# Optimization experiments

Measured on AMD Instinct MI355X. Metric: run time of the kernel, lower is better.

## Reference

```python
import jax, jax.numpy as jnp
import numpy as np

THETA = 10000.0
MASK_FILL = -60000.0

def _rope(x):
    # lucidrains rotary_embedding_torch semantics: interleaved pairs, full-dim rotation
    S, D = x.shape[-2], x.shape[-1]
    inv_freq = 1.0 / (THETA ** (jnp.arange(0, D, 2, dtype=jnp.float32) / D))  # [D/2]
    freqs = jnp.arange(S, dtype=jnp.float32)[:, None] * inv_freq[None, :]     # [S, D/2]
    freqs = jnp.repeat(freqs, 2, axis=-1)                                     # [S, D] (each freq twice)
    cos, sin = jnp.cos(freqs), jnp.sin(freqs)
    xr = x.reshape(x.shape[:-1] + (D // 2, 2))
    rot_half = jnp.stack((-xr[..., 1], xr[..., 0]), axis=-1).reshape(x.shape)  # (x1,x2)->(-x2,x1)
    return x * cos + rot_half * sin

def setup_inputs() -> dict:
    key = jax.random.key(0)
    kq, kk, kv, km = jax.random.split(key, 4)
    B, H, S, D = 4, 16, 2048, 128
    return {
        "query": jax.random.normal(kq, (B, H, S, D), dtype=jnp.float32),
        "key": jax.random.normal(kk, (B, H, S, D), dtype=jnp.float32),
        "value": jax.random.normal(kv, (B, H, S, D), dtype=jnp.float32),
        "mask": jax.random.randint(km, (1, 1, S, S), 0, 2, dtype=jnp.int32),
    }

def reference(query, key, value, mask):
    q = _rope(query)
    k = _rope(key)
    scale = 1.0 / jnp.sqrt(jnp.float32(q.shape[-1]))
    scores = jnp.einsum('bhqd,bhkd->bhqk', q, k) * scale
    scores = jnp.where(mask == 0, jnp.float32(MASK_FILL), scores)
    p_attn = jax.nn.softmax(scores, axis=-1)
    out = jnp.einsum('bhqk,bhkd->bhqd', p_attn, value)
    return out, p_attn
```

## Files before the change

### kernel.cpp

```cpp
#include <hip/hip_runtime.h>
#include <hip/hip_fp16.h>
#include <cstdint>
#include <cstddef>

#define Bn 4
#define Hn 16
#define Sn 2048
#define Dn 128
#define MSHIFT 8.0f

typedef _Float16 half8  __attribute__((ext_vector_type(8)));
typedef float    f32x16 __attribute__((ext_vector_type(16)));
typedef float    f32x4v __attribute__((ext_vector_type(4)));
typedef unsigned uint4v __attribute__((ext_vector_type(4)));

__device__ __forceinline__ int pk_f16(float a, float b){
  auto h = __builtin_amdgcn_cvt_pkrtz(a, b);
  return __builtin_bit_cast(int, h);
}


__global__ void k_prep0(float2* __restrict__ tab,
                        const int* __restrict__ mask, unsigned* __restrict__ mtb){
  const int bid = blockIdx.x;
  if (bid < 512){
    const int idx = bid*256 + threadIdx.x;
    const int i = idx & 63, s = idx >> 6;
    const double invf = exp(-(double)i * (9.210340371976184 / 64.0));
    const double ang  = (double)s * invf;
    float2 cs; cs.x = (float)cos(ang); cs.y = (float)sin(ang);
    tab[idx] = cs;
  } else {
    const int g = (bid - 512)*256 + threadIdx.x;
    const int k = g & (Sn-1), q32 = g >> 11;
    unsigned bits = 0u;
    for (int j = 0; j < 32; ++j)
      bits |= (mask[(size_t)(q32*32 + j)*Sn + k] != 0 ? 1u : 0u) << j;
    mtb[g] = bits;
  }
}


__global__ void k_pack(const float* __restrict__ q, const float* __restrict__ k,
                       const float* __restrict__ v, const float2* __restrict__ tab,
                       half8* __restrict__ qp, half8* __restrict__ kp,
                       half8* __restrict__ vp){
  const int bid = blockIdx.x;
  if (bid < 8192){
    const int t    = bid*256 + threadIdx.x;
    const int lane = t & 63, ln = lane & 31, h = lane >> 5;
    const int dc   = (t >> 6) & 7;
    const int blk  = (t >> 9) & 63;
    const int bh   = t >> 15;
    const int s    = blk*32 + ln;
    const size_t roff = ((size_t)bh*Sn + s)*Dn + dc*16 + h*8;
    const float4 a0 = *(const float4*)(q + roff);
    const float4 a1 = *(const float4*)(q + roff + 4);
    const float4 b0 = *(const float4*)(k + roff);
    const float4 b1 = *(const float4*)(k + roff + 4);
    const float2* tb = tab + s*64 + dc*8 + h*4;
    const float2 c0 = tb[0], c1 = tb[1], c2 = tb[2], c3 = tb[3];
    const float SC = 0.08838834764831845f;
    half8 qo, ko;
    qo[0] = (_Float16)((a0.x*c0.x - a0.y*c0.y)*SC);
    qo[1] = (_Float16)((a0.y*c0.x + a0.x*c0.y)*SC);
    qo[2] = (_Float16)((a0.z*c1.x - a0.w*c1.y)*SC);
    qo[3] = (_Float16)((a0.w*c1.x + a0.z*c1.y)*SC);
    qo[4] = (_Float16)((a1.x*c2.x - a1.y*c2.y)*SC);
    qo[5] = (_Float16)((a1.y*c2.x + a1.x*c2.y)*SC);
    qo[6] = (_Float16)((a1.z*c3.x - a1.w*c3.y)*SC);
    qo[7] = (_Float16)((a1.w*c3.x + a1.z*c3.y)*SC);
    ko[0] = (_Float16)(b0.x*c0.x - b0.y*c0.y);
    ko[1] = (_Float16)(b0.y*c0.x + b0.x*c0.y);
    ko[2] = (_Float16)(b0.z*c1.x - b0.w*c1.y);
    ko[3] = (_Float16)(b0.w*c1.x + b0.z*c1.y);
    ko[4] = (_Float16)(b1.x*c2.x - b1.y*c2.y);
    ko[5] = (_Float16)(b1.y*c2.x + b1.x*c2.y);
    ko[6] = (_Float16)(b1.z*c3.x - b1.w*c3.y);
    ko[7] = (_Float16)(b1.w*c3.x + b1.z*c3.y);
    qp[t] = qo;
    kp[t] = ko;
  } else {
    const int t    = (bid - 8192)*256 + threadIdx.x;
    const int lane = t & 63, ln = lane & 31, h = lane >> 5;
    const int dt   = (t >> 6) & 3;
    const int k16  = (t >> 8) & 127;
    const int bh   = t >> 15;
    const size_t base = ((size_t)bh*Sn + k16*16 + h*8)*Dn + dt*32 + ln;
    half8 o;
#pragma unroll
    for (int j = 0; j < 8; ++j) o[j] = (_Float16)v[base + (size_t)j*Dn];
    vp[t] = o;
  }
}


__global__ __launch_bounds__(512, 2) void attn_ps2(
    const half8* __restrict__ qp, const half8* __restrict__ kp,
    const unsigned* __restrict__ mtb, half8* __restrict__ wfrag,
    float* __restrict__ rinvb)
{
  const int bid  = blockIdx.x;
  const int work = ((bid & 7) << 6) + (bid >> 3);
  const int bh   = work >> 3;
  const int qg   = work & 7;
  const int w    = threadIdx.x >> 6;
  const int l    = threadIdx.x & 63;
  const int ln   = l & 31;
  const int h    = l >> 5;
  const int qb   = qg*8 + w;
  const int strip = bh*64 + qb;

  half8 qf[8];
#pragma unroll
  for (int dc = 0; dc < 8; ++dc)
    qf[dc] = qp[(((size_t)bh*64 + qb)*8 + dc)*64 + l];

  const unsigned* mrow = mtb + (size_t)qb*Sn;
  half8* wbase = wfrag + (size_t)strip*128*64;
  float L = 0.f;

  for (int kt = 0; kt < 64; ++kt){
    const half8* kf = kp + (((size_t)bh*64 + kt)*8)*64 + l;
    f32x16 a;
#pragma unroll
    for (int i = 0; i < 16; ++i) a[i] = 0.f;
#pragma unroll
    for (int dc = 0; dc < 8; ++dc)
      a = __builtin_amdgcn_mfma_f32_32x32x16_f16(kf[(size_t)dc*64], qf[dc], a, 0, 0, 0);

#pragma unroll
    for (int mm = 0; mm < 4; ++mm){
      const uint4v dw = *(const uint4v*)(mrow + kt*32 + mm*8 + h*4);
#pragma unroll
      for (int aa = 0; aa < 4; ++aa){
        const int r = mm*4 + aa;
        const float s = ((dw[aa] >> ln) & 1u) ? a[r] : -1.0e30f;
        const float u = __expf(s - MSHIFT);
        a[r] = u;
        L += u;
      }
    }

    int pk2[4][2];
#pragma unroll
    for (int b = 0; b < 4; ++b){
      pk2[b][0] = pk_f16(a[4*b+0], a[4*b+1]);
      pk2[b][1] = pk_f16(a[4*b+2], a[4*b+3]);
    }

#pragma unroll
    for (int t16 = 0; t16 < 2; ++t16){
      const int P00 = pk2[2*t16+0][0];
      const int P01 = pk2[2*t16+0][1];
      const int P10 = pk2[2*t16+1][0];
      const int P11 = pk2[2*t16+1][1];
      const int S00 = __shfl_xor(P00, 32, 64);
      const int S01 = __shfl_xor(P01, 32, 64);
      const int S10 = __shfl_xor(P10, 32, 64);
      const int S11 = __shfl_xor(P11, 32, 64);
      int4 bi;
      bi.x = h ? S10 : P00;
      bi.y = h ? S11 : P01;
      bi.z = h ? P10 : S00;
      bi.w = h ? P11 : S01;
      wbase[(size_t)(kt*2 + t16)*64 + l] = __builtin_bit_cast(half8, bi);
    }
  }

  L += __shfl_xor(L, 32, 64);
  if (l < 32) rinvb[(size_t)strip*32 + ln] = 1.0f / L;
}


__global__ __launch_bounds__(512, 2) void attn_ox(
    const half8* __restrict__ vp, const half8* __restrict__ wfrag,
    const float* __restrict__ rinvb, float* __restrict__ out,
    float* __restrict__ pout)
{
  __shared__ _Float16 ps[32][1032];
  __shared__ float rv[32];

  const int bid = blockIdx.x;
  const int tid = threadIdx.x;
  const int l   = tid & 63;
  const int ln  = l & 31;
  const int h   = l >> 5;

  if (bid % 17 == 0){
    const int o_id = bid / 17;
    const int work = 511 - (((o_id & 7) << 6) + (o_id >> 3));
    const int bh   = work >> 3;
    const int qg   = work & 7;
    const int w    = tid >> 6;
    const int qb   = qg*8 + w;
    const int strip = bh*64 + qb;
    float* pt = (float*)&ps[0][0];
    #define PT(W,Q,C) pt[(((W)*32 + (Q))*34) + (C)]

    f32x16 oacc[4];
#pragma unroll
    for (int dt = 0; dt < 4; ++dt)
#pragma unroll
      for (int i = 0; i < 16; ++i) oacc[dt][i] = 0.f;

    const half8* wbase = wfrag + (size_t)strip*128*64;
    const half8* vbase = vp + (size_t)bh*128*4*64;

#pragma unroll 4
    for (int ks = 0; ks < 128; ++ks){
      const half8 bf = wbase[(size_t)ks*64 + l];
      const half8* vf = vbase + (size_t)ks*4*64 + l;
#pragma unroll
      for (int dt = 0; dt < 4; ++dt)
        oacc[dt] = __builtin_amdgcn_mfma_f32_32x32x16_f16(vf[(size_t)dt*64], bf, oacc[dt], 0, 0, 0);
    }

    const float rinv = rinvb[(size_t)strip*32 + ln];
#pragma unroll
    for (int dt = 0; dt < 4; ++dt)
#pragma unroll
      for (int i = 0; i < 16; ++i) oacc[dt][i] *= rinv;

    const size_t obase = ((size_t)bh*Sn + qb*32)*Dn;
    const int rq = l >> 3;
    const int rc = (l & 7) * 4;
#pragma unroll
    for (int dt = 0; dt < 4; ++dt){
#pragma unroll
      for (int g = 0; g < 4; ++g){
        const int c = g*8 + h*4;
        float2 e0, e1;
        e0.x = oacc[dt][4*g+0]; e0.y = oacc[dt][4*g+1];
        e1.x = oacc[dt][4*g+2]; e1.y = oacc[dt][4*g+3];
        *(float2*)&PT(w, ln, c)   = e0;
        *(float2*)&PT(w, ln, c+2) = e1;
      }
#pragma unroll
      for (int i = 0; i < 4; ++i){
        const int qq = i*8 + rq;
        const float2 t0 = *(const float2*)&PT(w, qq, rc);
        const float2 t1 = *(const float2*)&PT(w, qq, rc+2);
        f32x4v o4; o4.x = t0.x; o4.y = t0.y; o4.z = t1.x; o4.w = t1.y;
        __builtin_nontemporal_store(o4, (f32x4v*)(out + obase + (size_t)qq*Dn + dt*32 + rc));
      }
    }
    #undef PT
  } else {
    const int e_id  = bid - bid/17 - 1;
    const int strip = e_id >> 1;
    const int hh    = e_id & 1;
    const int w8    = tid >> 6;

    if (tid < 32) rv[tid] = rinvb[(size_t)strip*32 + tid];

#pragma unroll
    for (int i = 0; i < 8; ++i){
      const int cc = w8*8 + i;
      const half8 v = wfrag[((size_t)strip*128 + hh*64 + cc)*64 + l];
      *(half8*)&ps[ln][cc*16 + h*8] = v;
    }
    __syncthreads();

    const int bh = strip >> 6, qb = strip & 63;
    float* dst0 = pout + ((size_t)bh*Sn + qb*32)*Sn + hh*1024;
#pragma unroll
    for (int it = 0; it < 8; ++it){
      const int id  = it*512 + tid;
      const int row = id >> 7;
      const int c   = (id & 127) * 8;
      const half8 hv = *(const half8*)&ps[row][c];
      const float r = rv[row];
      f32x4v v0, v1;
      v0.x = (float)hv[0]*r; v0.y = (float)hv[1]*r; v0.z = (float)hv[2]*r; v0.w = (float)hv[3]*r;
      v1.x = (float)hv[4]*r; v1.y = (float)hv[5]*r; v1.z = (float)hv[6]*r; v1.w = (float)hv[7]*r;
      float* dp = dst0 + (size_t)row*Sn + c;
      __builtin_nontemporal_store(v0, (f32x4v*)dp);
      __builtin_nontemporal_store(v1, (f32x4v*)(dp + 4));
    }
  }
}


extern "C" void kernel_launch(void* const* d_in, const int* in_sizes, int n_in,
                              void* d_out, int out_size, void* d_ws, size_t ws_size,
                              hipStream_t stream)
{
  const float* dq = (const float*)d_in[0];
  const float* dk = (const float*)d_in[1];
  const float* dv = (const float*)d_in[2];
  const int*   dm = (const int*)d_in[3];

  char* ws = (char*)d_ws;
  float2*   tab  = (float2*)ws;
  half8*    qp   = (half8*)(ws + (size_t)(1u<<20));
  half8*    kp   = (half8*)(ws + (size_t)(1u<<20) + ((size_t)32<<20));
  half8*    vp   = (half8*)(ws + (size_t)(1u<<20) + ((size_t)64<<20));
  unsigned* mtb  = (unsigned*)(ws + (size_t)(1u<<20) + ((size_t)96<<20));
  float*    rinvb= (float*)(ws + (size_t)(1u<<20) + ((size_t)97<<20));
  half8*    wfr  = (half8*)(ws + (size_t)(1u<<20) + ((size_t)98<<20));

  float* out  = (float*)d_out;
  float* pout = out + (size_t)Bn*Hn*Sn*Dn;

  k_prep0  <<<1024,  256, 0, stream>>>(tab, dm, mtb);
  k_pack   <<<16384, 256, 0, stream>>>(dq, dk, dv, tab, qp, kp, vp);
  attn_ps2 <<<512,   512, 0, stream>>>(qp, kp, mtb, wfr, rinvb);
  attn_ox  <<<8704,  512, 0, stream>>>(vp, wfr, rinvb, out, pout);
}
```

Baseline: 893.9 us.

## Co-schedule V packing with the score/exp kernel to overlap compute and memory

The V fp16 packing leaves k_pack and now runs inside the score kernel, where one block in nine does the MFMA score/exp strip and the other eight convert V. The aim is to hide the bandwidth-bound V conversion behind the compute-bound QK^T/exp work and shorten k_pack. The output kernel's strip order also changes from a reversed interleave to plain sequential. Interleaving mixed block types may disturb occupancy or scheduling balance.

Result: faster. 845.7 us, median of 2 (-5.4%).

```diff
diff --git a/kernel.cpp b/kernel.cpp
--- a/kernel.cpp
+++ b/kernel.cpp
@@ -42,46 +42,127 @@
 
 
 __global__ void k_pack(const float* __restrict__ q, const float* __restrict__ k,
-                       const float* __restrict__ v, const float2* __restrict__ tab,
-                       half8* __restrict__ qp, half8* __restrict__ kp,
-                       half8* __restrict__ vp){
+                       const float2* __restrict__ tab,
+                       half8* __restrict__ qp, half8* __restrict__ kp){
+  const int t    = blockIdx.x*256 + threadIdx.x;
+  const int lane = t & 63, ln = lane & 31, h = lane >> 5;
+  const int dc   = (t >> 6) & 7;
+  const int blk  = (t >> 9) & 63;
+  const int bh   = t >> 15;
+  const int s    = blk*32 + ln;
+  const size_t roff = ((size_t)bh*Sn + s)*Dn + dc*16 + h*8;
+  const float4 a0 = *(const float4*)(q + roff);
+  const float4 a1 = *(const float4*)(q + roff + 4);
+  const float4 b0 = *(const float4*)(k + roff);
+  const float4 b1 = *(const float4*)(k + roff + 4);
+  const float2* tb = tab + s*64 + dc*8 + h*4;
+  const float2 c0 = tb[0], c1 = tb[1], c2 = tb[2], c3 = tb[3];
+  const float SC = 0.08838834764831845f;
+  half8 qo, ko;
+  qo[0] = (_Float16)((a0.x*c0.x - a0.y*c0.y)*SC);
+  qo[1] = (_Float16)((a0.y*c0.x + a0.x*c0.y)*SC);
+  qo[2] = (_Float16)((a0.z*c1.x - a0.w*c1.y)*SC);
+  qo[3] = (_Float16)((a0.w*c1.x + a0.z*c1.y)*SC);
+  qo[4] = (_Float16)((a1.x*c2.x - a1.y*c2.y)*SC);
+  qo[5] = (_Float16)((a1.y*c2.x + a1.x*c2.y)*SC);
+  qo[6] = (_Float16)((a1.z*c3.x - a1.w*c3.y)*SC);
+  qo[7] = (_Float16)((a1.w*c3.x + a1.z*c3.y)*SC);
+  ko[0] = (_Float16)(b0.x*c0.x - b0.y*c0.y);
+  ko[1] = (_Float16)(b0.y*c0.x + b0.x*c0.y);
+  ko[2] = (_Float16)(b0.z*c1.x - b0.w*c1.y);
+  ko[3] = (_Float16)(b0.w*c1.x + b0.z*c1.y);
+  ko[4] = (_Float16)(b1.x*c2.x - b1.y*c2.y);
+  ko[5] = (_Float16)(b1.y*c2.x + b1.x*c2.y);
+  ko[6] = (_Float16)(b1.z*c3.x - b1.w*c3.y);
+  ko[7] = (_Float16)(b1.w*c3.x + b1.z*c3.y);
+  qp[t] = qo;
+  kp[t] = ko;
+}
+
+
+__global__ __launch_bounds__(512, 2) void attn_psv(
+    const half8* __restrict__ qp, const half8* __restrict__ kp,
+    const unsigned* __restrict__ mtb, const float* __restrict__ v,
+    half8* __restrict__ wfrag, float* __restrict__ rinvb,
+    half8* __restrict__ vp)
+{
   const int bid = blockIdx.x;
-  if (bid < 8192){
-    const int t    = bid*256 + threadIdx.x;
-    const int lane = t & 63, ln = lane & 31, h = lane >> 5;
-    const int dc   = (t >> 6) & 7;
-    const int blk  = (t >> 9) & 63;
-    const int bh   = t >> 15;
-    const int s    = blk*32 + ln;
-    const size_t roff = ((size_t)bh*Sn + s)*Dn + dc*16 + h*8;
-    const float4 a0 = *(const float4*)(q + roff);
-    const float4 a1 = *(const float4*)(q + roff + 4);
-    const float4 b0 = *(const float4*)(k + roff);
-    const float4 b1 = *(const float4*)(k + roff + 4);
-    const float2* tb = tab + s*64 + dc*8 + h*4;
-    const float2 c0 = tb[0], c1 = tb[1], c2 = tb[2], c3 = tb[3];
-    const float SC = 0.08838834764831845f;
-    half8 qo, ko;
-    qo[0] = (_Float16)((a0.x*c0.x - a0.y*c0.y)*SC);
-    qo[1] = (_Float16)((a0.y*c0.x + a0.x*c0.y)*SC);
-    qo[2] = (_Float16)((a0.z*c1.x - a0.w*c1.y)*SC);
-    qo[3] = (_Float16)((a0.w*c1.x + a0.z*c1.y)*SC);
-    qo[4] = (_Float16)((a1.x*c2.x - a1.y*c2.y)*SC);
-    qo[5] = (_Float16)((a1.y*c2.x + a1.x*c2.y)*SC);
-    qo[6] = (_Float16)((a1.z*c3.x - a1.w*c3.y)*SC);
-    qo[7] = (_Float16)((a1.w*c3.x + a1.z*c3.y)*SC);
-    ko[0] = (_Float16)(b0.x*c0.x - b0.y*c0.y);
-    ko[1] = (_Float16)(b0.y*c0.x + b0.x*c0.y);
-    ko[2] = (_Float16)(b0.z*c1.x - b0.w*c1.y);
-    ko[3] = (_Float16)(b0.w*c1.x + b0.z*c1.y);
-    ko[4] = (_Float16)(b1.x*c2.x - b1.y*c2.y);
-    ko[5] = (_Float16)(b1.y*c2.x + b1.x*c2.y);
-    ko[6] = (_Float16)(b1.z*c3.x - b1.w*c3.y);
-    ko[7] = (_Float16)(b1.w*c3.x + b1.z*c3.y);
-    qp[t] = qo;
-    kp[t] = ko;
+  const int tid = threadIdx.x;
+
+  if (bid % 9 == 0){
+    const int p_id = bid / 9;
+    const int work = ((p_id & 7) << 6) + (p_id >> 3);
+    const int bh   = work >> 3;
+    const int qg   = work & 7;
+    const int w    = tid >> 6;
+    const int l    = tid & 63;
+    const int ln   = l & 31;
+    const int h    = l >> 5;
+    const int qb   = qg*8 + w;
+    const int strip = bh*64 + qb;
+
+    half8 qf[8];
+#pragma unroll
+    for (int dc = 0; dc < 8; ++dc)
+      qf[dc] = qp[(((size_t)bh*64 + qb)*8 + dc)*64 + l];
+
+    const unsigned* mrow = mtb + (size_t)qb*Sn;
+    half8* wbase = wfrag + (size_t)strip*128*64;
+    float L = 0.f;
+
+    for (int kt = 0; kt < 64; ++kt){
+      const half8* kf = kp + (((size_t)bh*64 + kt)*8)*64 + l;
+      f32x16 a;
+#pragma unroll
+      for (int i = 0; i < 16; ++i) a[i] = 0.f;
+#pragma unroll
+      for (int dc = 0; dc < 8; ++dc)
+        a = __builtin_amdgcn_mfma_f32_32x32x16_f16(kf[(size_t)dc*64], qf[dc], a, 0, 0, 0);
+
+#pragma unroll
+      for (int mm = 0; mm < 4; ++mm){
+        const uint4v dw = *(const uint4v*)(mrow + kt*32 + mm*8 + h*4);
+#pragma unroll
+        for (int aa = 0; aa < 4; ++aa){
+          const int r = mm*4 + aa;
+          const float s = ((dw[aa] >> ln) & 1u) ? a[r] : -1.0e30f;
+          const float u = __expf(s - MSHIFT);
+          a[r] = u;
+          L += u;
+        }
+      }
+
+      int pk2[4][2];
+#pragma unroll
+      for (int b = 0; b < 4; ++b){
+        pk2[b][0] = pk_f16(a[4*b+0], a[4*b+1]);
+        pk2[b][1] = pk_f16(a[4*b+2], a[4*b+3]);
+      }
+
+#pragma unroll
+      for (int t16 = 0; t16 < 2; ++t16){
+        const int P00 = pk2[2*t16+0][0];
+        const int P01 = pk2[2*t16+0][1];
+        const int P10 = pk2[2*t16+1][0];
+        const int P11 = pk2[2*t16+1][1];
+        const int S00 = __shfl_xor(P00, 32, 64);
+        const int S01 = __shfl_xor(P01, 32, 64);
+        const int S10 = __shfl_xor(P10, 32, 64);
+        const int S11 = __shfl_xor(P11, 32, 64);
+        int4 bi;
+        bi.x = h ? S10 : P00;
+        bi.y = h ? S11 : P01;
+        bi.z = h ? P10 : S00;
+        bi.w = h ? P11 : S01;
+        wbase[(size_t)(kt*2 + t16)*64 + l] = __builtin_bit_cast(half8, bi);
+      }
+    }
+
+    L += __shfl_xor(L, 32, 64);
+    if (l < 32) rinvb[(size_t)strip*32 + ln] = 1.0f / L;
   } else {
-    const int t    = (bid - 8192)*256 + threadIdx.x;
+    const int v_id = bid - bid/9 - 1;
+    const int t    = v_id*512 + tid;
     const int lane = t & 63, ln = lane & 31, h = lane >> 5;
     const int dt   = (t >> 6) & 3;
     const int k16  = (t >> 8) & 127;
@@ -92,84 +173,6 @@
     for (int j = 0; j < 8; ++j) o[j] = (_Float16)v[base + (size_t)j*Dn];
     vp[t] = o;
   }
-}
-
-
-__global__ __launch_bounds__(512, 2) void attn_ps2(
-    const half8* __restrict__ qp, const half8* __restrict__ kp,
-    const unsigned* __restrict__ mtb, half8* __restrict__ wfrag,
-    float* __restrict__ rinvb)
-{
-  const int bid  = blockIdx.x;
-  const int work = ((bid & 7) << 6) + (bid >> 3);
-  const int bh   = work >> 3;
-  const int qg   = work & 7;
-  const int w    = threadIdx.x >> 6;
-  const int l    = threadIdx.x & 63;
-  const int ln   = l & 31;
-  const int h    = l >> 5;
-  const int qb   = qg*8 + w;
-  const int strip = bh*64 + qb;
-
-  half8 qf[8];
-#pragma unroll
-  for (int dc = 0; dc < 8; ++dc)
-    qf[dc] = qp[(((size_t)bh*64 + qb)*8 + dc)*64 + l];
-
-  const unsigned* mrow = mtb + (size_t)qb*Sn;
-  half8* wbase = wfrag + (size_t)strip*128*64;
-  float L = 0.f;
-
-  for (int kt = 0; kt < 64; ++kt){
-    const half8* kf = kp + (((size_t)bh*64 + kt)*8)*64 + l;
-    f32x16 a;
-#pragma unroll
-    for (int i = 0; i < 16; ++i) a[i] = 0.f;
-#pragma unroll
-    for (int dc = 0; dc < 8; ++dc)
-      a = __builtin_amdgcn_mfma_f32_32x32x16_f16(kf[(size_t)dc*64], qf[dc], a, 0, 0, 0);
-
-#pragma unroll
-    for (int mm = 0; mm < 4; ++mm){
-      const uint4v dw = *(const uint4v*)(mrow + kt*32 + mm*8 + h*4);
-#pragma unroll
-      for (int aa = 0; aa < 4; ++aa){
-        const int r = mm*4 + aa;
-        const float s = ((dw[aa] >> ln) & 1u) ? a[r] : -1.0e30f;
-        const float u = __expf(s - MSHIFT);
-        a[r] = u;
-        L += u;
-      }
-    }
-
-    int pk2[4][2];
-#pragma unroll
-    for (int b = 0; b < 4; ++b){
-      pk2[b][0] = pk_f16(a[4*b+0], a[4*b+1]);
-      pk2[b][1] = pk_f16(a[4*b+2], a[4*b+3]);
-    }
-
-#pragma unroll
-    for (int t16 = 0; t16 < 2; ++t16){
-      const int P00 = pk2[2*t16+0][0];
-      const int P01 = pk2[2*t16+0][1];
-      const int P10 = pk2[2*t16+1][0];
-      const int P11 = pk2[2*t16+1][1];
-      const int S00 = __shfl_xor(P00, 32, 64);
-      const int S01 = __shfl_xor(P01, 32, 64);
-      const int S10 = __shfl_xor(P10, 32, 64);
-      const int S11 = __shfl_xor(P11, 32, 64);
-      int4 bi;
-      bi.x = h ? S10 : P00;
-      bi.y = h ? S11 : P01;
-      bi.z = h ? P10 : S00;
-      bi.w = h ? P11 : S01;
-      wbase[(size_t)(kt*2 + t16)*64 + l] = __builtin_bit_cast(half8, bi);
-    }
-  }
-
-  L += __shfl_xor(L, 32, 64);
-  if (l < 32) rinvb[(size_t)strip*32 + ln] = 1.0f / L;
 }
 
 
@@ -188,8 +191,7 @@
   const int h   = l >> 5;
 
   if (bid % 17 == 0){
-    const int o_id = bid / 17;
-    const int work = 511 - (((o_id & 7) << 6) + (o_id >> 3));
+    const int work = bid / 17;
     const int bh   = work >> 3;
     const int qg   = work & 7;
     const int w    = tid >> 6;
@@ -303,8 +305,8 @@
   float* out  = (float*)d_out;
   float* pout = out + (size_t)Bn*Hn*Sn*Dn;
 
-  k_prep0  <<<1024,  256, 0, stream>>>(tab, dm, mtb);
-  k_pack   <<<16384, 256, 0, stream>>>(dq, dk, dv, tab, qp, kp, vp);
-  attn_ps2 <<<512,   512, 0, stream>>>(qp, kp, mtb, wfr, rinvb);
-  attn_ox  <<<8704,  512, 0, stream>>>(vp, wfr, rinvb, out, pout);
-}
+  k_prep0  <<<1024, 256, 0, stream>>>(tab, dm, mtb);
+  k_pack   <<<8192, 256, 0, stream>>>(dq, dk, tab, qp, kp);
+  attn_psv <<<4608, 512, 0, stream>>>(qp, kp, mtb, dv, wfr, rinvb, vp);
+  attn_ox  <<<8704, 512, 0, stream>>>(vp, wfr, rinvb, out, pout);
+}
```
